# Kernel optimization log

Measured on AMD Instinct MI355X. Metric: run time of the kernel, lower is better.

The kernel has to match this reference:

```python
import jax, jax.numpy as jnp
import numpy as np

B, L, C = 2, 384, 128
H, DK, NQP, NPV = 8, 16, 4, 8
WC = float(np.sqrt(2.0 / (9.0 * NQP)))
WL = float(np.sqrt(1.0 / 3.0))


def setup_inputs() -> dict:
    key = jax.random.key(0)
    ks = jax.random.split(key, 16)
    s = 0.02
    inp = {
        "si": jax.random.normal(ks[0], (B, L, C), jnp.float32),
        "zij": jax.random.normal(ks[1], (B, L, L, C), jnp.float32),
        "Ri": jax.random.normal(ks[2], (B, L, 3, 3), jnp.float32),
        "Ti": jax.random.normal(ks[3], (B, L, 3, 1), jnp.float32),
        "WQh": jax.random.normal(ks[4], (C, H * DK), jnp.float32) * s,
        "WKh": jax.random.normal(ks[5], (C, H * DK), jnp.float32) * s,
        "WVh": jax.random.normal(ks[6], (C, H * DK), jnp.float32) * s,
        "WQhp": jax.random.normal(ks[7], (C, H * NQP * 3), jnp.float32) * s,
        "WKhp": jax.random.normal(ks[8], (C, H * NQP * 3), jnp.float32) * s,
        "WVhp": jax.random.normal(ks[9], (C, H * NPV * 3), jnp.float32) * s,
        "Wb": jax.random.normal(ks[10], (C, H), jnp.float32) * s,
        "WOw": jax.random.normal(ks[11], (H * C + H * DK + H * NPV * 3 + H * NPV, C), jnp.float32) * s,
        "WOb": jnp.zeros((C,), jnp.float32),
        "gamah": jnp.zeros((H,), jnp.float32),
    }
    return inp


def reference(si, zij, Ri, Ti, WQh, WKh, WVh, WQhp, WKhp, WVhp, Wb, WOw, WOb, gamah):
    b, l, c = si.shape
    t = Ti[..., 0]  # [B,L,3]

    # scalar q/k/v: [B,L,H,DK]
    q = (si @ WQh).reshape(b, l, H, DK)
    k = (si @ WKh).reshape(b, l, H, DK)
    v = (si @ WVh).reshape(b, l, H, DK)

    # pair bias: [B,H,L,L]
    bij = jnp.einsum("bijc,ch->bhij", zij, Wb)
    scores1 = jnp.einsum("bihd,bjhd->bhij", q, k) / np.sqrt(DK) + bij

    # query/key points, rigid-transformed: [B,L,H,P,3]
    qp = (si @ WQhp).reshape(b, l, H, NQP, 3)
    kp = (si @ KHP_shape_fix(WKhp)).reshape(b, l, H, NQP, 3) if False else (si @ WKhp).reshape(b, l, H, NQP, 3)
    qpt = jnp.einsum("bixy,bihpy->bihpx", Ri, qp) + t[:, :, None, None, :]
    kpt = jnp.einsum("bixy,bihpy->bihpx", Ri, kp) + t[:, :, None, None, :]

    # squared point distances summed over points and coords, via |q|^2+|k|^2-2qk
    sq_q = jnp.sum(qpt * qpt, axis=(-1, -2))  # [B,L,H]
    sq_k = jnp.sum(kpt * kpt, axis=(-1, -2))  # [B,L,H]
    dot = jnp.einsum("bihpx,bjhpx->bhij", qpt, kpt)
    d2 = sq_q.transpose(0, 2, 1)[:, :, :, None] + sq_k.transpose(0, 2, 1)[:, :, None, :] - 2.0 * dot

    scores2 = jax.nn.softplus(gamah)[None, :, None, None] * (WC / 2.0) * d2
    scores = WL * (scores1 - scores2)
    alphah = jax.nn.softmax(scores, axis=3)  # [B,H,L,L]

    # pair-rep aggregation: [B,L,H,C]
    o_pair = jnp.einsum("bhij,bijc->bihc", alphah, zij)
    # scalar value attention: [B,L,H,DK]
    o_val = jnp.einsum("bhij,bjhd->bihd", alphah, v)

    # point values, transformed, attended, then inverse-transformed
    vp = (si @ WVhp).reshape(b, l, H, NPV, 3)
    vpt = jnp.einsum("bjxy,bjhpy->bjhpx", Ri, vp) + t[:, :, None, None, :]
    opt = jnp.einsum("bhij,bjhpx->bihpx", alphah, vpt)  # [B,L,H,NPV,3]
    ohp = jnp.einsum("binm,bihpn->bihpm", Ri, opt - t[:, :, None, None, :])  # R^T (o - t)

    feats = jnp.concatenate(
        [
            o_pair.reshape(b, l, H * c),
            o_val.reshape(b, l, H * DK),
            ohp.reshape(b, l, H * NPV * 3),
            jnp.abs(ohp).sum(axis=-1).reshape(b, l, H * NPV),
        ],
        axis=2,
    )
    return feats @ WOw + WOb


def KHP_shape_fix(w):  # unused placeholder kept for readability of the conditional above
    return w
```

## Files before the change

kernel.cpp:

```cpp
#include <hip/hip_runtime.h>
#include <hip/hip_bf16.h>

#define Bq 2
#define Lq 384
#define Cq 128
#define Hq 8

static constexpr float WCH   = 0.11785113019775792f;
static constexpr float WLc   = 0.5773502691896258f;
static constexpr float LOG2E = 1.4426950408889634f;

typedef __attribute__((ext_vector_type(8))) short bf16x8;
typedef __attribute__((ext_vector_type(4))) float f32x4;

__device__ __forceinline__ unsigned short f2bf(float f) {
  __hip_bfloat16 h = __float2bfloat16(f);
  unsigned short u; __builtin_memcpy(&u, &h, 2); return u;
}
__device__ __forceinline__ unsigned packbf(float a, float b) {
  return (unsigned)f2bf(a) | ((unsigned)f2bf(b) << 16);
}
__device__ __forceinline__ float bf2f(unsigned short u) {
  unsigned x = ((unsigned)u) << 16; float f; __builtin_memcpy(&f, &x, 4); return f;
}
__device__ __forceinline__ bf16x8 ld_frag(const unsigned* p) {
  union { bf16x8 v; unsigned u[4]; } x;
  x.u[0] = p[0]; x.u[1] = p[1]; x.u[2] = p[2]; x.u[3] = p[3];
  return x.v;
}

#define BAR() asm volatile("s_waitcnt lgkmcnt(0)\ns_barrier" ::: "memory")

__global__ __launch_bounds__(256) void k_proj(
    const float* __restrict__ si,
    const float* __restrict__ WQh, const float* __restrict__ WKh, const float* __restrict__ WVh,
    const float* __restrict__ WQhp, const float* __restrict__ WKhp, const float* __restrict__ WVhp,
    float* __restrict__ q, float* __restrict__ k, float* __restrict__ v,
    float* __restrict__ raw)
{
  __shared__ unsigned sm[4352*2];
  unsigned* at = sm;
  unsigned* bt = sm + 4352;
  unsigned short* bt16 = (unsigned short*)bt;
  const int t = threadIdx.x;
  const int tb = blockIdx.x / 12, ct = blockIdx.x % 12;
  const int tok0 = tb*64, cg0 = ct*64;

  {
    const float4* sp = (const float4*)si;
    #pragma unroll
    for (int rep = 0; rep < 8; ++rep) {
      int idx = rep*256 + t;
      int tl = idx >> 5, cq = idx & 31;
      float4 vv = sp[(size_t)(tok0+tl)*32 + cq];
      uint2 u; u.x = packbf(vv.x, vv.y); u.y = packbf(vv.z, vv.w);
      *(uint2*)(&at[tl*68 + cq*2]) = u;
    }
  }
  {
    const int cq = t & 15;
    const int cg = cg0 + cq*4;
    const float* Wsrc; int ncol, coff;
    if (cg < 128)      { Wsrc = WQh; ncol = 128; coff = cg; }
    else if (cg < 256) { Wsrc = WKh; ncol = 128; coff = cg-128; }
    else if (cg < 384) { Wsrc = WVh; ncol = 128; coff = cg-256; }
    else { int pc = cg-384;
      if (pc < 96)       { Wsrc = WQhp; ncol = 96;  coff = pc; }
      else if (pc < 192) { Wsrc = WKhp; ncol = 96;  coff = pc-96; }
      else               { Wsrc = WVhp; ncol = 192; coff = pc-192; } }
    #pragma unroll
    for (int rep = 0; rep < 8; ++rep) {
      int c = rep*16 + (t >> 4);
      float4 wv = *(const float4*)(Wsrc + (size_t)c*ncol + coff);
      bt16[(cq*4+0)*136 + c] = f2bf(wv.x);
      bt16[(cq*4+1)*136 + c] = f2bf(wv.y);
      bt16[(cq*4+2)*136 + c] = f2bf(wv.z);
      bt16[(cq*4+3)*136 + c] = f2bf(wv.w);
    }
  }
  __syncthreads();
  const int l = t & 63, w = t >> 6, g = l >> 4, n16 = l & 15;
  bf16x8 afr[4];
  #pragma unroll
  for (int ks = 0; ks < 4; ++ks)
    afr[ks] = ld_frag(&at[(w*16 + n16)*68 + ks*16 + g*4]);
  f32x4 acc[4];
  #pragma unroll
  for (int nl = 0; nl < 4; ++nl) { acc[nl][0]=0.f; acc[nl][1]=0.f; acc[nl][2]=0.f; acc[nl][3]=0.f; }
  #pragma unroll
  for (int nl = 0; nl < 4; ++nl)
    #pragma unroll
    for (int ks = 0; ks < 4; ++ks) {
      bf16x8 bfr = ld_frag(&bt[(nl*16 + n16)*68 + ks*16 + g*4]);
      acc[nl] = __builtin_amdgcn_mfma_f32_16x16x32_bf16(afr[ks], bfr, acc[nl], 0, 0, 0);
    }
  if (ct < 6) {
    float* dst = (ct < 2) ? q : (ct < 4) ? k : v;
    int colbase = cg0 - (ct >> 1)*128;
    #pragma unroll
    for (int nl = 0; nl < 4; ++nl)
      #pragma unroll
      for (int r = 0; r < 4; ++r)
        dst[(size_t)(tok0 + w*16 + g*4 + r)*128 + colbase + nl*16 + n16] = acc[nl][r];
  } else {
    int pcb = cg0 - 384;
    #pragma unroll
    for (int nl = 0; nl < 4; ++nl)
      #pragma unroll
      for (int r = 0; r < 4; ++r)
        raw[(size_t)(tok0 + w*16 + g*4 + r)*384 + pcb + nl*16 + n16] = acc[nl][r];
  }
}

__global__ __launch_bounds__(256) void k_xform(
    const float* __restrict__ raw, const float* __restrict__ Ri, const float* __restrict__ Ti,
    const float* __restrict__ qg, const float* __restrict__ kg, const float* __restrict__ gamah,
    float* __restrict__ vpt, unsigned* __restrict__ apk, unsigned* __restrict__ bpk)
{
  __shared__ float ssq[128];
  __shared__ float spt[2][64][3];
  __shared__ float smsq[2][2][8];
  const int t = threadIdx.x;
  const int tk = t >> 7, pt = t & 127;
  const int tok = blockIdx.x*2 + tk;
  {
    const float* R = Ri + tok*9;
    const float* T = Ti + tok*3;
    int ro = (pt < 32) ? pt*3 : (pt < 64) ? 96 + (pt-32)*3 : 192 + (pt-64)*3;
    float x0 = raw[(size_t)tok*384 + ro + 0], x1 = raw[(size_t)tok*384 + ro + 1], x2 = raw[(size_t)tok*384 + ro + 2];
    float o0 = T[0] + R[0]*x0 + R[1]*x1 + R[2]*x2;
    float o1 = T[1] + R[3]*x0 + R[4]*x1 + R[5]*x2;
    float o2 = T[2] + R[6]*x0 + R[7]*x1 + R[8]*x2;
    if (pt >= 64) {
      int doff = tok*192 + (pt-64)*3;
      vpt[doff] = o0; vpt[doff+1] = o1; vpt[doff+2] = o2;
    } else {
      spt[tk][pt][0] = o0; spt[tk][pt][1] = o1; spt[tk][pt][2] = o2;
      ssq[tk*64 + pt] = o0*o0 + o1*o1 + o2*o2;
    }
  }
  __syncthreads();
  if (t < 32) {
    int tk2 = t >> 4, r = t & 15, isK = r >> 3, h = r & 7;
    int base = tk2*64 + isK*32 + h*4;
    smsq[tk2][isK][h] = ssq[base] + ssq[base+1] + ssq[base+2] + ssq[base+3];
  }
  __syncthreads();
  {
    const int ab = t >> 7, rem = t & 127;
    const int tk2 = rem >> 6, h = (rem >> 3) & 7, d0 = (t & 7)*2;
    const int tokg = blockIdx.x*2 + tk2;
    float gv = gamah[h];
    float sp = (gv > 20.f) ? gv : log1pf(__expf(gv));
    float c1 = WLc*0.25f, c2 = 2.f*WLc*sp*WCH, c3 = WLc*sp*WCH;
    unsigned* dst = (ab ? bpk : apk) + ((size_t)tokg*8 + h)*16;
    #pragma unroll
    for (int dd = 0; dd < 2; ++dd) {
      int dw = d0 + dd;
      float vv[2];
      #pragma unroll
      for (int e = 0; e < 2; ++e) {
        int kk = dw*2 + e;
        float val;
        if (kk < 16)      val = (ab ? kg : qg)[(size_t)tokg*128 + h*16 + kk] * (ab ? 1.f : c1);
        else if (kk < 28) { int pi = kk-16;
                            float cv = spt[tk2][ab*32 + h*4 + pi/3][pi%3];
                            val = ab ? cv : cv*c2; }
        else if (kk == 28) val = ab ? 1.f : -c3*smsq[tk2][0][h];
        else if (kk == 29) val = ab ? smsq[tk2][1][h] : -c3;
        else               val = 0.f;
        vv[e] = val;
      }
      dst[dw] = packbf(vv[0], vv[1]);
    }
  }
}

__global__ __launch_bounds__(256) void k_geom(
    const unsigned* __restrict__ apk, const unsigned* __restrict__ bpk,
    float* __restrict__ g)
{
  __shared__ unsigned bt[384*20];
  const int t = threadIdx.x;
  const int bh = blockIdx.x / 6, ib = blockIdx.x % 6;
  const int b = bh >> 3, h = bh & 7, i0 = ib*64;
  #pragma unroll
  for (int rep = 0; rep < 6; ++rep) {
    int idx = rep*256 + t;
    int j = idx >> 2, dq = idx & 3;
    uint4 vv = *(const uint4*)(bpk + ((size_t)(b*Lq + j)*8 + h)*16 + dq*4);
    *(uint4*)(&bt[j*20 + dq*4]) = vv;
  }
  __syncthreads();
  const int l = t & 63, w = t >> 6, g2 = l >> 4, n16 = l & 15;
  union { uint4 u; bf16x8 v; } au;
  au.u = *(const uint4*)(apk + ((size_t)(b*Lq + i0 + w*16 + n16)*8 + h)*16 + g2*4);
  bf16x8 afr = au.v;
  float* grow = g + (size_t)(b*8 + h)*Lq*Lq;
  for (int jt = 0; jt < 24; ++jt) {
    bf16x8 bfr = ld_frag(&bt[(jt*16 + n16)*20 + g2*4]);
    f32x4 acc = {0.f,0.f,0.f,0.f};
    acc = __builtin_amdgcn_mfma_f32_16x16x32_bf16(afr, bfr, acc, 0, 0, 0);
    #pragma unroll
    for (int r = 0; r < 4; ++r)
      grow[(size_t)(i0 + w*16 + g2*4 + r)*Lq + jt*16 + n16] = acc[r];
  }
}

#define ZS   0
#define ZT   4352
#define GS   8832
#define P2O  11936
#define WBT  12496
#define WMX  13568
#define LSM  13632
#define SCL  13696
#define INV  13704
#define OPTS 13712
#define OS   13904
#define SMTOT 14928

__global__ __launch_bounds__(256, 2) void k_attn(
    const float* __restrict__ zij, const float* __restrict__ gmat,
    const float* __restrict__ v, const float* __restrict__ vpt,
    const float* __restrict__ Wb, const float* __restrict__ Ri, const float* __restrict__ Ti,
    float* __restrict__ feats)
{
  __shared__ unsigned sm[SMTOT];
  float* smf = (float*)sm;
  const int t = threadIdx.x;
  const int bx = blockIdx.x;
  const int b = bx / Lq, i = bx % Lq;
  const int tok = bx;
  const int l = t & 63, w = t >> 6, g = l >> 4, hh = l & 15;

  {
    const float* gp = gmat + (size_t)(b*8)*Lq*Lq + (size_t)i*Lq;
    #pragma unroll
    for (int rep = 0; rep < 3; ++rep) {
      int idx = rep*256 + t;
      int h2 = idx / 96, jq = idx % 96;
      float4 gv = *(const float4*)(gp + (size_t)h2*Lq*Lq + jq*4);
      *(float4*)(&smf[GS + h2*388 + jq*4]) = gv;
    }
    unsigned short* wb16 = (unsigned short*)(sm + WBT);
    #pragma unroll
    for (int rep = 0; rep < 8; ++rep) {
      int idx = rep*256 + t;
      int h2 = idx >> 7, c = idx & 127;
      wb16[h2*134 + c] = (h2 < 8) ? f2bf(Wb[c*8 + h2]) : (unsigned short)0;
    }
  }
  __syncthreads();
  bf16x8 wbf[4];
  #pragma unroll
  for (int ks = 0; ks < 4; ++ks) wbf[ks] = ld_frag(&sm[WBT + hh*67 + ks*16 + g*4]);

  f32x4 opacc0 = {0.f,0.f,0.f,0.f}, opacc1 = {0.f,0.f,0.f,0.f};
  float m_run = -1e30f, l_run = 0.f;
  float va0 = 0.f, va1 = 0.f;
  int role_h = 0; const float* rp = nullptr; int rstride = 0;
  if (t < 64)       { role_h = t >> 3; rp = v   + (size_t)b*Lq*128 + role_h*16 + (t & 7)*2; rstride = 128; }
  else if (t < 160) { int qq = t - 64; role_h = qq / 12;
                      rp = vpt + (size_t)b*Lq*192 + role_h*24 + (qq % 12)*2; rstride = 192; }

  const int c4 = t & 31, jr = t >> 5;
  const float4* zp = (const float4*)(zij + (size_t)tok*Lq*128);
  unsigned short* zt16 = (unsigned short*)(sm + ZT);
  float4 zr[8];
  #pragma unroll
  for (int pp = 0; pp < 8; ++pp) zr[pp] = zp[(size_t)(pp*8 + jr)*32 + c4];

  for (int ch = 0; ch < 6; ++ch) {
    const int j0 = ch*64;
    BAR();
    #pragma unroll
    for (int pp = 0; pp < 8; ++pp) {
      int j = pp*8 + jr;
      uint2 u; u.x = packbf(zr[pp].x, zr[pp].y); u.y = packbf(zr[pp].z, zr[pp].w);
      *(uint2*)(&sm[ZS + j*68 + c4*2]) = u;
      zt16[(c4*4+0)*70 + j] = (unsigned short)(u.x & 0xffffu);
      zt16[(c4*4+1)*70 + j] = (unsigned short)(u.x >> 16);
      zt16[(c4*4+2)*70 + j] = (unsigned short)(u.y & 0xffffu);
      zt16[(c4*4+3)*70 + j] = (unsigned short)(u.y >> 16);
    }
    if (ch < 5) {
      #pragma unroll
      for (int pp = 0; pp < 8; ++pp)
        zr[pp] = zp[(size_t)(j0 + 64 + pp*8 + jr)*32 + c4];
    }
    BAR();
    f32x4 bij = {0.f,0.f,0.f,0.f};
    #pragma unroll
    for (int ks = 0; ks < 4; ++ks) {
      bf16x8 a = ld_frag(&sm[ZS + (w*16 + hh)*68 + ks*16 + g*4]);
      bij = __builtin_amdgcn_mfma_f32_16x16x32_bf16(a, wbf[ks], bij, 0, 0, 0);
    }
    float s0, s1, s2, s3;
    if (hh < 8) {
      f32x4 gq = *(const f32x4*)(&smf[GS + hh*388 + j0 + w*16 + g*4]);
      s0 = gq[0] + WLc*bij[0]; s1 = gq[1] + WLc*bij[1];
      s2 = gq[2] + WLc*bij[2]; s3 = gq[3] + WLc*bij[3];
    } else { s0 = s1 = s2 = s3 = -1e30f; }
    float m4 = fmaxf(fmaxf(s0,s1), fmaxf(s2,s3));
    m4 = fmaxf(m4, __shfl_xor(m4, 16));
    m4 = fmaxf(m4, __shfl_xor(m4, 32));
    if (l < 16) smf[WMX + w*16 + l] = m4;
    BAR();
    float cmax = fmaxf(fmaxf(smf[WMX+hh], smf[WMX+16+hh]),
                       fmaxf(smf[WMX+32+hh], smf[WMX+48+hh]));
    float m_new = fmaxf(m_run, cmax);
    float sc = exp2f((m_run - m_new)*LOG2E);
    m_run = m_new;
    float p0 = exp2f((s0 - m_new)*LOG2E);
    float p1 = exp2f((s1 - m_new)*LOG2E);
    float p2 = exp2f((s2 - m_new)*LOG2E);
    float p3 = exp2f((s3 - m_new)*LOG2E);
    float psum = p0+p1+p2+p3;
    psum += __shfl_xor(psum, 16);
    psum += __shfl_xor(psum, 32);
    l_run = l_run*sc + psum;
    sm[P2O + hh*35 + w*8 + g*2    ] = packbf(p0, p1);
    sm[P2O + hh*35 + w*8 + g*2 + 1] = packbf(p2, p3);
    opacc0 = opacc0 * sc;
    opacc1 = opacc1 * sc;
    if (w == 0 && l < 8) smf[SCL + l] = sc;
    BAR();
    #pragma unroll
    for (int ks = 0; ks < 2; ++ks) {
      bf16x8 bb = ld_frag(&sm[P2O + hh*35 + ks*16 + g*4]);
      bf16x8 a0 = ld_frag(&sm[ZT + ((w  )*16 + hh)*35 + ks*16 + g*4]);
      bf16x8 a1 = ld_frag(&sm[ZT + ((w+4)*16 + hh)*35 + ks*16 + g*4]);
      opacc0 = __builtin_amdgcn_mfma_f32_16x16x32_bf16(a0, bb, opacc0, 0, 0, 0);
      opacc1 = __builtin_amdgcn_mfma_f32_16x16x32_bf16(a1, bb, opacc1, 0, 0, 0);
    }
    if (t < 160) {
      float scl = smf[SCL + role_h];
      va0 *= scl; va1 *= scl;
      #pragma unroll 4
      for (int jj = 0; jj < 64; jj += 2) {
        unsigned pw = sm[P2O + role_h*35 + (jj>>1)];
        float pa = bf2f((unsigned short)(pw & 0xffffu));
        float pb = bf2f((unsigned short)(pw >> 16));
        const float* pj = rp + (size_t)(j0+jj)*rstride;
        const float* pk2 = pj + rstride;
        va0 += pa*pj[0] + pb*pk2[0];
        va1 += pa*pj[1] + pb*pk2[1];
      }
    }
  }
  __syncthreads();
  if (l < 16) smf[LSM + w*16 + l] = l_run;
  __syncthreads();
  if (t < 8) {
    float lt = smf[LSM+t] + smf[LSM+16+t] + smf[LSM+32+t] + smf[LSM+48+t];
    smf[INV + t] = 1.f / lt;
  }
  __syncthreads();
  const size_t fb = (size_t)tok * 1408;
  if (hh < 8) {
    float inv = smf[INV + hh];
    #pragma unroll
    for (int r = 0; r < 4; ++r) {
      smf[OS + hh*128 + (w  )*16 + g*4 + r] = opacc0[r]*inv;
      smf[OS + hh*128 + (w+4)*16 + g*4 + r] = opacc1[r]*inv;
    }
  }
  if (t < 64) {
    float inv = smf[INV + role_h];
    int off = role_h*16 + (t & 7)*2;
    feats[fb + 1024 + off    ] = va0*inv;
    feats[fb + 1024 + off + 1] = va1*inv;
  } else if (t < 160) {
    float inv = smf[INV + role_h];
    int qq = t - 64;
    smf[OPTS + role_h*24 + (qq%12)*2    ] = va0*inv;
    smf[OPTS + role_h*24 + (qq%12)*2 + 1] = va1*inv;
  }
  __syncthreads();
  for (int rep = 0; rep < 4; ++rep) {
    int idx = rep*256 + t;
    feats[fb + idx] = smf[OS + idx];
  }
  if (t < 64) {
    int h2 = t >> 3, p = t & 7;
    const float* R = Ri + tok*9;
    const float* T = Ti + tok*3;
    float ox = smf[OPTS + h2*24 + p*3 + 0] - T[0];
    float oy = smf[OPTS + h2*24 + p*3 + 1] - T[1];
    float oz = smf[OPTS + h2*24 + p*3 + 2] - T[2];
    float r0 = R[0]*ox + R[3]*oy + R[6]*oz;
    float r1 = R[1]*ox + R[4]*oy + R[7]*oz;
    float r2 = R[2]*ox + R[5]*oy + R[8]*oz;
    feats[fb + 1152 + (h2*8+p)*3 + 0] = r0;
    feats[fb + 1152 + (h2*8+p)*3 + 1] = r1;
    feats[fb + 1152 + (h2*8+p)*3 + 2] = r2;
    feats[fb + 1344 + h2*8 + p] = fabsf(r0) + fabsf(r1) + fabsf(r2);
  }
}

__global__ __launch_bounds__(256) void k_out(
    const float* __restrict__ feats, const float* __restrict__ WOw,
    const float* __restrict__ WOb, float* __restrict__ out)
{
  __shared__ float sf[8448];
  const int t = threadIdx.x;
  const int r0 = blockIdx.x * 6;
  for (int rep = 0; rep < 33; ++rep) {
    int idx = rep*256 + t;
    int row = idx / 1408, f = idx % 1408;
    sf[f*6 + row] = feats[(size_t)(r0+row)*1408 + f];
  }
  __syncthreads();
  const int c4 = t & 31, fq = t >> 5;
  float acc[6][4];
  #pragma unroll
  for (int r = 0; r < 6; ++r)
    #pragma unroll
    for (int e = 0; e < 4; ++e) acc[r][e] = 0.f;
  const float* wp = WOw + (size_t)fq*176*128 + c4*4;
  for (int f = 0; f < 176; ++f) {
    const f32x4 wv = *(const f32x4*)(wp + (size_t)f*128);
    int fg = fq*176 + f;
    float fv[6];
    #pragma unroll
    for (int r = 0; r < 6; ++r) fv[r] = sf[fg*6 + r];
    #pragma unroll
    for (int r = 0; r < 6; ++r)
      #pragma unroll
      for (int e = 0; e < 4; ++e) acc[r][e] += fv[r]*wv[e];
  }
  __syncthreads();
  #pragma unroll
  for (int r = 0; r < 6; ++r)
    #pragma unroll
    for (int e = 0; e < 4; ++e)
      sf[(fq*6 + r)*128 + c4*4 + e] = acc[r][e];
  __syncthreads();
  for (int rep = 0; rep < 3; ++rep) {
    int idx = rep*256 + t;
    int r = idx >> 7, cc = idx & 127;
    float s = 0.f;
    #pragma unroll
    for (int fq2 = 0; fq2 < 8; ++fq2) s += sf[(fq2*6 + r)*128 + cc];
    out[(size_t)(r0+r)*128 + cc] = s + WOb[cc];
  }
}

extern "C" void kernel_launch(void* const* d_in, const int* in_sizes, int n_in,
                              void* d_out, int out_size, void* d_ws, size_t ws_size,
                              hipStream_t stream) {
  const float* si    = (const float*)d_in[0];
  const float* zij   = (const float*)d_in[1];
  const float* Ri    = (const float*)d_in[2];
  const float* Ti    = (const float*)d_in[3];
  const float* WQh   = (const float*)d_in[4];
  const float* WKh   = (const float*)d_in[5];
  const float* WVh   = (const float*)d_in[6];
  const float* WQhp  = (const float*)d_in[7];
  const float* WKhp  = (const float*)d_in[8];
  const float* WVhp  = (const float*)d_in[9];
  const float* Wb    = (const float*)d_in[10];
  const float* WOw   = (const float*)d_in[11];
  const float* WOb   = (const float*)d_in[12];
  const float* gamah = (const float*)d_in[13];

  float* ws   = (float*)d_ws;
  float* q    = ws;
  float* k    = q    + 98304;
  float* v    = k    + 98304;
  float* vpt  = v    + 98304;
  float* raw  = vpt  + 147456;
  float* g    = raw  + 294912;
  float* feats= g    + 2359296;
  unsigned* apk = (unsigned*)feats;
  unsigned* bpk = apk + 98304;
  float* out  = (float*)d_out;

  k_proj <<<144, 256, 0, stream>>>(si, WQh, WKh, WVh, WQhp, WKhp, WVhp, q, k, v, raw);
  k_xform<<<384, 256, 0, stream>>>(raw, Ri, Ti, q, k, gamah, vpt, apk, bpk);
  k_geom <<<96,  256, 0, stream>>>(apk, bpk, g);
  k_attn <<<768, 256, 0, stream>>>(zij, g, v, vpt, Wb, Ri, Ti, feats);
  k_out  <<<128, 256, 0, stream>>>(feats, WOw, WOb, out);
}
```

Measured before the change: 314.4 us.

## Move value and point-value attention onto fp16 MFMA with transposed staged operands

Every matrix op switches from bf16 to fp16 MFMA. The scalar-value and point-value aggregation in the attention kernel moves from per-thread scalar FMA loops over global memory onto MFMA. To feed it, v and the transformed value points are written as transposed fp16 arrays, prefetched per chunk alongside zij and staged in shared memory. The pair-bias g rows are now held in registers instead of shared memory, and per-row softmax rescale factors are tracked for the new accumulators. This aims to remove the scalar global-load bottleneck in k_attn, at the cost of more registers and shared memory, and fp16 range and precision risk.

```diff
diff --git a/kernel.cpp b/kernel.cpp
--- a/kernel.cpp
+++ b/kernel.cpp
@@ -10,21 +10,18 @@
 static constexpr float WLc   = 0.5773502691896258f;
 static constexpr float LOG2E = 1.4426950408889634f;
 
-typedef __attribute__((ext_vector_type(8))) short bf16x8;
+typedef __fp16 f16x8 __attribute__((ext_vector_type(8)));
 typedef __attribute__((ext_vector_type(4))) float f32x4;
 
-__device__ __forceinline__ unsigned short f2bf(float f) {
-  __hip_bfloat16 h = __float2bfloat16(f);
-  unsigned short u; __builtin_memcpy(&u, &h, 2); return u;
-}
-__device__ __forceinline__ unsigned packbf(float a, float b) {
-  return (unsigned)f2bf(a) | ((unsigned)f2bf(b) << 16);
-}
-__device__ __forceinline__ float bf2f(unsigned short u) {
-  unsigned x = ((unsigned)u) << 16; float f; __builtin_memcpy(&f, &x, 4); return f;
-}
-__device__ __forceinline__ bf16x8 ld_frag(const unsigned* p) {
-  union { bf16x8 v; unsigned u[4]; } x;
+__device__ __forceinline__ unsigned short f2h(float f) {
+  __fp16 h = (__fp16)f; unsigned short u; __builtin_memcpy(&u, &h, 2); return u;
+}
+__device__ __forceinline__ unsigned packh(float a, float b) {
+  auto v = __builtin_amdgcn_cvt_pkrtz(a, b);
+  unsigned u; __builtin_memcpy(&u, &v, 4); return u;
+}
+__device__ __forceinline__ f16x8 ld_frag16(const unsigned* p) {
+  union { f16x8 v; unsigned u[4]; } x;
   x.u[0] = p[0]; x.u[1] = p[1]; x.u[2] = p[2]; x.u[3] = p[3];
   return x.v;
 }
@@ -35,7 +32,7 @@
     const float* __restrict__ si,
     const float* __restrict__ WQh, const float* __restrict__ WKh, const float* __restrict__ WVh,
     const float* __restrict__ WQhp, const float* __restrict__ WKhp, const float* __restrict__ WVhp,
-    float* __restrict__ q, float* __restrict__ k, float* __restrict__ v,
+    float* __restrict__ q, float* __restrict__ k, unsigned short* __restrict__ vt_g,
     float* __restrict__ raw)
 {
   __shared__ unsigned sm[4352*2];
@@ -53,7 +50,7 @@
       int idx = rep*256 + t;
       int tl = idx >> 5, cq = idx & 31;
       float4 vv = sp[(size_t)(tok0+tl)*32 + cq];
-      uint2 u; u.x = packbf(vv.x, vv.y); u.y = packbf(vv.z, vv.w);
+      uint2 u; u.x = packh(vv.x, vv.y); u.y = packh(vv.z, vv.w);
       *(uint2*)(&at[tl*68 + cq*2]) = u;
     }
   }
@@ -72,18 +69,18 @@
     for (int rep = 0; rep < 8; ++rep) {
       int c = rep*16 + (t >> 4);
       float4 wv = *(const float4*)(Wsrc + (size_t)c*ncol + coff);
-      bt16[(cq*4+0)*136 + c] = f2bf(wv.x);
-      bt16[(cq*4+1)*136 + c] = f2bf(wv.y);
-      bt16[(cq*4+2)*136 + c] = f2bf(wv.z);
-      bt16[(cq*4+3)*136 + c] = f2bf(wv.w);
+      bt16[(cq*4+0)*136 + c] = f2h(wv.x);
+      bt16[(cq*4+1)*136 + c] = f2h(wv.y);
+      bt16[(cq*4+2)*136 + c] = f2h(wv.z);
+      bt16[(cq*4+3)*136 + c] = f2h(wv.w);
     }
   }
   __syncthreads();
   const int l = t & 63, w = t >> 6, g = l >> 4, n16 = l & 15;
-  bf16x8 afr[4];
+  f16x8 afr[4];
   #pragma unroll
   for (int ks = 0; ks < 4; ++ks)
-    afr[ks] = ld_frag(&at[(w*16 + n16)*68 + ks*16 + g*4]);
+    afr[ks] = ld_frag16(&at[(w*16 + n16)*68 + ks*16 + g*4]);
   f32x4 acc[4];
   #pragma unroll
   for (int nl = 0; nl < 4; ++nl) { acc[nl][0]=0.f; acc[nl][1]=0.f; acc[nl][2]=0.f; acc[nl][3]=0.f; }
@@ -91,17 +88,24 @@
   for (int nl = 0; nl < 4; ++nl)
     #pragma unroll
     for (int ks = 0; ks < 4; ++ks) {
-      bf16x8 bfr = ld_frag(&bt[(nl*16 + n16)*68 + ks*16 + g*4]);
-      acc[nl] = __builtin_amdgcn_mfma_f32_16x16x32_bf16(afr[ks], bfr, acc[nl], 0, 0, 0);
-    }
-  if (ct < 6) {
-    float* dst = (ct < 2) ? q : (ct < 4) ? k : v;
+      f16x8 bfr = ld_frag16(&bt[(nl*16 + n16)*68 + ks*16 + g*4]);
+      acc[nl] = __builtin_amdgcn_mfma_f32_16x16x32_f16(afr[ks], bfr, acc[nl], 0, 0, 0);
+    }
+  if (ct < 4) {
+    float* dst = (ct < 2) ? q : k;
     int colbase = cg0 - (ct >> 1)*128;
     #pragma unroll
     for (int nl = 0; nl < 4; ++nl)
       #pragma unroll
       for (int r = 0; r < 4; ++r)
         dst[(size_t)(tok0 + w*16 + g*4 + r)*128 + colbase + nl*16 + n16] = acc[nl][r];
+  } else if (ct < 6) {
+    int colbase = cg0 - 256;
+    #pragma unroll
+    for (int nl = 0; nl < 4; ++nl)
+      #pragma unroll
+      for (int r = 0; r < 4; ++r)
+        vt_g[(size_t)(colbase + nl*16 + n16)*768 + tok0 + w*16 + g*4 + r] = f2h(acc[nl][r]);
   } else {
     int pcb = cg0 - 384;
     #pragma unroll
@@ -115,7 +119,7 @@
 __global__ __launch_bounds__(256) void k_xform(
     const float* __restrict__ raw, const float* __restrict__ Ri, const float* __restrict__ Ti,
     const float* __restrict__ qg, const float* __restrict__ kg, const float* __restrict__ gamah,
-    float* __restrict__ vpt, unsigned* __restrict__ apk, unsigned* __restrict__ bpk)
+    unsigned short* __restrict__ vptt, unsigned* __restrict__ apk, unsigned* __restrict__ bpk)
 {
   __shared__ float ssq[128];
   __shared__ float spt[2][64][3];
@@ -132,8 +136,10 @@
     float o1 = T[1] + R[3]*x0 + R[4]*x1 + R[5]*x2;
     float o2 = T[2] + R[6]*x0 + R[7]*x1 + R[8]*x2;
     if (pt >= 64) {
-      int doff = tok*192 + (pt-64)*3;
-      vpt[doff] = o0; vpt[doff+1] = o1; vpt[doff+2] = o2;
+      int col = (pt-64)*3;
+      vptt[(size_t)(col+0)*768 + tok] = f2h(o0);
+      vptt[(size_t)(col+1)*768 + tok] = f2h(o1);
+      vptt[(size_t)(col+2)*768 + tok] = f2h(o2);
     } else {
       spt[tk][pt][0] = o0; spt[tk][pt][1] = o1; spt[tk][pt][2] = o2;
       ssq[tk*64 + pt] = o0*o0 + o1*o1 + o2*o2;
@@ -171,7 +177,7 @@
         else               val = 0.f;
         vv[e] = val;
       }
-      dst[dw] = packbf(vv[0], vv[1]);
+      dst[dw] = packh(vv[0], vv[1]);
     }
   }
 }
@@ -193,122 +199,161 @@
   }
   __syncthreads();
   const int l = t & 63, w = t >> 6, g2 = l >> 4, n16 = l & 15;
-  union { uint4 u; bf16x8 v; } au;
+  union { uint4 u; f16x8 v; } au;
   au.u = *(const uint4*)(apk + ((size_t)(b*Lq + i0 + w*16 + n16)*8 + h)*16 + g2*4);
-  bf16x8 afr = au.v;
+  f16x8 afr = au.v;
   float* grow = g + (size_t)(b*8 + h)*Lq*Lq;
   for (int jt = 0; jt < 24; ++jt) {
-    bf16x8 bfr = ld_frag(&bt[(jt*16 + n16)*20 + g2*4]);
+    f16x8 bfr = ld_frag16(&bt[(jt*16 + n16)*20 + g2*4]);
     f32x4 acc = {0.f,0.f,0.f,0.f};
-    acc = __builtin_amdgcn_mfma_f32_16x16x32_bf16(afr, bfr, acc, 0, 0, 0);
+    acc = __builtin_amdgcn_mfma_f32_16x16x32_f16(afr, bfr, acc, 0, 0, 0);
     #pragma unroll
     for (int r = 0; r < 4; ++r)
       grow[(size_t)(i0 + w*16 + g2*4 + r)*Lq + jt*16 + n16] = acc[r];
   }
 }
 
-#define ZS   0
-#define ZT   4352
-#define GS   8832
-#define P2O  11936
-#define WBT  12496
-#define WMX  13568
-#define LSM  13632
-#define SCL  13696
-#define INV  13704
-#define OPTS 13712
-#define OS   13904
-#define SMTOT 14928
+#define ZSo   0
+#define ZTo   4224
+#define VTo   8704
+#define VPo   12928
+#define P2o   19264
+#define WBo   19824
+#define WMo   20368
+#define INVo  20432
+#define SMTOT 20440
+#define OPo   0
+#define OSo   8704
 
 __global__ __launch_bounds__(256, 2) void k_attn(
     const float* __restrict__ zij, const float* __restrict__ gmat,
-    const float* __restrict__ v, const float* __restrict__ vpt,
+    const unsigned short* __restrict__ vt_g, const unsigned short* __restrict__ vptt,
     const float* __restrict__ Wb, const float* __restrict__ Ri, const float* __restrict__ Ti,
     float* __restrict__ feats)
 {
   __shared__ unsigned sm[SMTOT];
   float* smf = (float*)sm;
+  unsigned short* zt16 = (unsigned short*)(sm + ZTo);
   const int t = threadIdx.x;
   const int bx = blockIdx.x;
   const int b = bx / Lq, i = bx % Lq;
-  const int tok = bx;
   const int l = t & 63, w = t >> 6, g = l >> 4, hh = l & 15;
 
+  const int c4 = t & 31, jr = t >> 5;
+  const float4* zp = (const float4*)(zij + (size_t)bx*Lq*128);
+  float4 zr[8];
+  #pragma unroll
+  for (int pp = 0; pp < 8; ++pp) zr[pp] = zp[(size_t)(pp*8 + jr)*32 + c4];
+  const uint4* vtp = (const uint4*)vt_g;
+  const uint4* vpp = (const uint4*)vptt;
+  uint4 vtr[4], vpr[6];
+  #pragma unroll
+  for (int q2 = 0; q2 < 4; ++q2) {
+    int u = q2*256 + t, row = u >> 3, seg = u & 7;
+    vtr[q2] = vtp[row*96 + b*48 + seg];
+  }
+  #pragma unroll
+  for (int q2 = 0; q2 < 6; ++q2) {
+    int u = q2*256 + t, row = u >> 3, seg = u & 7;
+    vpr[q2] = vpp[row*96 + b*48 + seg];
+  }
+
+  f32x4 greg[6];
+  #pragma unroll
+  for (int ch = 0; ch < 6; ++ch) { greg[ch][0]=0.f; greg[ch][1]=0.f; greg[ch][2]=0.f; greg[ch][3]=0.f; }
+  if (hh < 8) {
+    const float* gp = gmat + ((size_t)(b*8 + hh)*Lq + i)*Lq;
+    #pragma unroll
+    for (int ch = 0; ch < 6; ++ch)
+      greg[ch] = *(const f32x4*)(gp + ch*64 + w*16 + g*4);
+  }
+
   {
-    const float* gp = gmat + (size_t)(b*8)*Lq*Lq + (size_t)i*Lq;
-    #pragma unroll
-    for (int rep = 0; rep < 3; ++rep) {
+    unsigned short* wb16 = (unsigned short*)(sm + WBo);
+    #pragma unroll
+    for (int rep = 0; rep < 4; ++rep) {
       int idx = rep*256 + t;
-      int h2 = idx / 96, jq = idx % 96;
-      float4 gv = *(const float4*)(gp + (size_t)h2*Lq*Lq + jq*4);
-      *(float4*)(&smf[GS + h2*388 + jq*4]) = gv;
-    }
-    unsigned short* wb16 = (unsigned short*)(sm + WBT);
-    #pragma unroll
-    for (int rep = 0; rep < 8; ++rep) {
-      int idx = rep*256 + t;
-      int h2 = idx >> 7, c = idx & 127;
-      wb16[h2*134 + c] = (h2 < 8) ? f2bf(Wb[c*8 + h2]) : (unsigned short)0;
-    }
-  }
-  __syncthreads();
-  bf16x8 wbf[4];
-  #pragma unroll
-  for (int ks = 0; ks < 4; ++ks) wbf[ks] = ld_frag(&sm[WBT + hh*67 + ks*16 + g*4]);
+      int c = idx >> 3, h2 = idx & 7;
+      wb16[h2*136 + c] = f2h(Wb[c*8 + h2]);
+    }
+  }
+  __syncthreads();
+  const f16x8 zf8 = {0,0,0,0,0,0,0,0};
+  f16x8 wbf[4];
+  #pragma unroll
+  for (int ks = 0; ks < 4; ++ks)
+    wbf[ks] = (hh < 8) ? ld_frag16(&sm[WBo + hh*68 + ks*16 + g*4]) : zf8;
 
   f32x4 opacc0 = {0.f,0.f,0.f,0.f}, opacc1 = {0.f,0.f,0.f,0.f};
+  f32x4 anv0 = {0.f,0.f,0.f,0.f}, anv1 = {0.f,0.f,0.f,0.f};
+  f32x4 apv0 = {0.f,0.f,0.f,0.f}, apv1 = {0.f,0.f,0.f,0.f}, apv2 = {0.f,0.f,0.f,0.f};
   float m_run = -1e30f, l_run = 0.f;
-  float va0 = 0.f, va1 = 0.f;
-  int role_h = 0; const float* rp = nullptr; int rstride = 0;
-  if (t < 64)       { role_h = t >> 3; rp = v   + (size_t)b*Lq*128 + role_h*16 + (t & 7)*2; rstride = 128; }
-  else if (t < 160) { int qq = t - 64; role_h = qq / 12;
-                      rp = vpt + (size_t)b*Lq*192 + role_h*24 + (qq % 12)*2; rstride = 192; }
-
-  const int c4 = t & 31, jr = t >> 5;
-  const float4* zp = (const float4*)(zij + (size_t)tok*Lq*128);
-  unsigned short* zt16 = (unsigned short*)(sm + ZT);
-  float4 zr[8];
-  #pragma unroll
-  for (int pp = 0; pp < 8; ++pp) zr[pp] = zp[(size_t)(pp*8 + jr)*32 + c4];
+  float mr0 = -1e30f, mr1 = -1e30f, mr2 = -1e30f, mr3 = -1e30f;
 
   for (int ch = 0; ch < 6; ++ch) {
-    const int j0 = ch*64;
     BAR();
     #pragma unroll
     for (int pp = 0; pp < 8; ++pp) {
       int j = pp*8 + jr;
-      uint2 u; u.x = packbf(zr[pp].x, zr[pp].y); u.y = packbf(zr[pp].z, zr[pp].w);
-      *(uint2*)(&sm[ZS + j*68 + c4*2]) = u;
-      zt16[(c4*4+0)*70 + j] = (unsigned short)(u.x & 0xffffu);
-      zt16[(c4*4+1)*70 + j] = (unsigned short)(u.x >> 16);
-      zt16[(c4*4+2)*70 + j] = (unsigned short)(u.y & 0xffffu);
-      zt16[(c4*4+3)*70 + j] = (unsigned short)(u.y >> 16);
+      unsigned u0 = packh(zr[pp].x, zr[pp].y), u1 = packh(zr[pp].z, zr[pp].w);
+      uint2 u; u.x = u0; u.y = u1;
+      *(uint2*)(&sm[ZSo + j*66 + c4*2]) = u;
+      zt16[(c4*4+0)*70 + j] = (unsigned short)(u0 & 0xffffu);
+      zt16[(c4*4+1)*70 + j] = (unsigned short)(u0 >> 16);
+      zt16[(c4*4+2)*70 + j] = (unsigned short)(u1 & 0xffffu);
+      zt16[(c4*4+3)*70 + j] = (unsigned short)(u1 >> 16);
+    }
+    #pragma unroll
+    for (int q2 = 0; q2 < 4; ++q2) {
+      int u = q2*256 + t, row = u >> 3, seg = u & 7;
+      sm[VTo + row*33 + seg*4    ] = vtr[q2].x;
+      sm[VTo + row*33 + seg*4 + 1] = vtr[q2].y;
+      sm[VTo + row*33 + seg*4 + 2] = vtr[q2].z;
+      sm[VTo + row*33 + seg*4 + 3] = vtr[q2].w;
+    }
+    #pragma unroll
+    for (int q2 = 0; q2 < 6; ++q2) {
+      int u = q2*256 + t, row = u >> 3, seg = u & 7;
+      sm[VPo + row*33 + seg*4    ] = vpr[q2].x;
+      sm[VPo + row*33 + seg*4 + 1] = vpr[q2].y;
+      sm[VPo + row*33 + seg*4 + 2] = vpr[q2].z;
+      sm[VPo + row*33 + seg*4 + 3] = vpr[q2].w;
     }
     if (ch < 5) {
+      int j0n = (ch+1)*64;
       #pragma unroll
       for (int pp = 0; pp < 8; ++pp)
-        zr[pp] = zp[(size_t)(j0 + 64 + pp*8 + jr)*32 + c4];
+        zr[pp] = zp[(size_t)(j0n + pp*8 + jr)*32 + c4];
+      #pragma unroll
+      for (int q2 = 0; q2 < 4; ++q2) {
+        int u = q2*256 + t, row = u >> 3, seg = u & 7;
+        vtr[q2] = vtp[row*96 + b*48 + (ch+1)*8 + seg];
+      }
+      #pragma unroll
+      for (int q2 = 0; q2 < 6; ++q2) {
+        int u = q2*256 + t, row = u >> 3, seg = u & 7;
+        vpr[q2] = vpp[row*96 + b*48 + (ch+1)*8 + seg];
+      }
     }
     BAR();
     f32x4 bij = {0.f,0.f,0.f,0.f};
     #pragma unroll
     for (int ks = 0; ks < 4; ++ks) {
-      bf16x8 a = ld_frag(&sm[ZS + (w*16 + hh)*68 + ks*16 + g*4]);
-      bij = __builtin_amdgcn_mfma_f32_16x16x32_bf16(a, wbf[ks], bij, 0, 0, 0);
+      f16x8 a = ld_frag16(&sm[ZSo + (w*16 + hh)*66 + ks*16 + g*4]);
+      bij = __builtin_amdgcn_mfma_f32_16x16x32_f16(a, wbf[ks], bij, 0, 0, 0);
     }
     float s0, s1, s2, s3;
     if (hh < 8) {
-      f32x4 gq = *(const f32x4*)(&smf[GS + hh*388 + j0 + w*16 + g*4]);
-      s0 = gq[0] + WLc*bij[0]; s1 = gq[1] + WLc*bij[1];
-      s2 = gq[2] + WLc*bij[2]; s3 = gq[3] + WLc*bij[3];
+      s0 = greg[ch][0] + WLc*bij[0]; s1 = greg[ch][1] + WLc*bij[1];
+      s2 = greg[ch][2] + WLc*bij[2]; s3 = greg[ch][3] + WLc*bij[3];
     } else { s0 = s1 = s2 = s3 = -1e30f; }
     float m4 = fmaxf(fmaxf(s0,s1), fmaxf(s2,s3));
     m4 = fmaxf(m4, __shfl_xor(m4, 16));
     m4 = fmaxf(m4, __shfl_xor(m4, 32));
-    if (l < 16) smf[WMX + w*16 + l] = m4;
+    if (l < 16) smf[WMo + w*16 + l] = m4;
     BAR();
-    float cmax = fmaxf(fmaxf(smf[WMX+hh], smf[WMX+16+hh]),
-                       fmaxf(smf[WMX+32+hh], smf[WMX+48+hh]));
+    float cmax = fmaxf(fmaxf(smf[WMo+hh], smf[WMo+16+hh]),
+                       fmaxf(smf[WMo+32+hh], smf[WMo+48+hh]));
     float m_new = fmaxf(m_run, cmax);
     float sc = exp2f((m_run - m_new)*LOG2E);
     m_run = m_new;
@@ -320,75 +365,99 @@
     psum += __shfl_xor(psum, 16);
     psum += __shfl_xor(psum, 32);
     l_run = l_run*sc + psum;
-    sm[P2O + hh*35 + w*8 + g*2    ] = packbf(p0, p1);
-    sm[P2O + hh*35 + w*8 + g*2 + 1] = packbf(p2, p3);
+    sm[P2o + hh*35 + w*8 + g*2    ] = packh(p0, p1);
+    sm[P2o + hh*35 + w*8 + g*2 + 1] = packh(p2, p3);
+    float scr0, scr1, scr2, scr3;
+    {
+      int hr = g*4;
+      float cm, mn;
+      cm = fmaxf(fmaxf(smf[WMo+hr], smf[WMo+16+hr]), fmaxf(smf[WMo+32+hr], smf[WMo+48+hr]));
+      mn = fmaxf(mr0, cm); scr0 = exp2f((mr0 - mn)*LOG2E); mr0 = mn;
+      cm = fmaxf(fmaxf(smf[WMo+hr+1], smf[WMo+17+hr]), fmaxf(smf[WMo+33+hr], smf[WMo+49+hr]));
+      mn = fmaxf(mr1, cm); scr1 = exp2f((mr1 - mn)*LOG2E); mr1 = mn;
+      cm = fmaxf(fmaxf(smf[WMo+hr+2], smf[WMo+18+hr]), fmaxf(smf[WMo+34+hr], smf[WMo+50+hr]));
+      mn = fmaxf(mr2, cm); scr2 = exp2f((mr2 - mn)*LOG2E); mr2 = mn;
+      cm = fmaxf(fmaxf(smf[WMo+hr+3], smf[WMo+19+hr]), fmaxf(smf[WMo+35+hr], smf[WMo+51+hr]));
+      mn = fmaxf(mr3, cm); scr3 = exp2f((mr3 - mn)*LOG2E); mr3 = mn;
+    }
     opacc0 = opacc0 * sc;
     opacc1 = opacc1 * sc;
-    if (w == 0 && l < 8) smf[SCL + l] = sc;
+    anv0[0]*=scr0; anv0[1]*=scr1; anv0[2]*=scr2; anv0[3]*=scr3;
+    anv1[0]*=scr0; anv1[1]*=scr1; anv1[2]*=scr2; anv1[3]*=scr3;
+    apv0[0]*=scr0; apv0[1]*=scr1; apv0[2]*=scr2; apv0[3]*=scr3;
+    apv1[0]*=scr0; apv1[1]*=scr1; apv1[2]*=scr2; apv1[3]*=scr3;
+    apv2[0]*=scr0; apv2[1]*=scr1; apv2[2]*=scr2; apv2[3]*=scr3;
     BAR();
     #pragma unroll
     for (int ks = 0; ks < 2; ++ks) {
-      bf16x8 bb = ld_frag(&sm[P2O + hh*35 + ks*16 + g*4]);
-      bf16x8 a0 = ld_frag(&sm[ZT + ((w  )*16 + hh)*35 + ks*16 + g*4]);
-      bf16x8 a1 = ld_frag(&sm[ZT + ((w+4)*16 + hh)*35 + ks*16 + g*4]);
-      opacc0 = __builtin_amdgcn_mfma_f32_16x16x32_bf16(a0, bb, opacc0, 0, 0, 0);
-      opacc1 = __builtin_amdgcn_mfma_f32_16x16x32_bf16(a1, bb, opacc1, 0, 0, 0);
-    }
-    if (t < 160) {
-      float scl = smf[SCL + role_h];
-      va0 *= scl; va1 *= scl;
-      #pragma unroll 4
-      for (int jj = 0; jj < 64; jj += 2) {
-        unsigned pw = sm[P2O + role_h*35 + (jj>>1)];
-        float pa = bf2f((unsigned short)(pw & 0xffffu));
-        float pb = bf2f((unsigned short)(pw >> 16));
-        const float* pj = rp + (size_t)(j0+jj)*rstride;
-        const float* pk2 = pj + rstride;
-        va0 += pa*pj[0] + pb*pk2[0];
-        va1 += pa*pj[1] + pb*pk2[1];
-      }
-    }
-  }
-  __syncthreads();
-  if (l < 16) smf[LSM + w*16 + l] = l_run;
+      f16x8 bb = ld_frag16(&sm[P2o + hh*35 + ks*16 + g*4]);
+      f16x8 a0 = ld_frag16(&sm[ZTo + ((w  )*16 + hh)*35 + ks*16 + g*4]);
+      f16x8 a1 = ld_frag16(&sm[ZTo + ((w+4)*16 + hh)*35 + ks*16 + g*4]);
+      opacc0 = __builtin_amdgcn_mfma_f32_16x16x32_f16(a0, bb, opacc0, 0, 0, 0);
+      opacc1 = __builtin_amdgcn_mfma_f32_16x16x32_f16(a1, bb, opacc1, 0, 0, 0);
+      f16x8 v0 = ld_frag16(&sm[VTo + ((2*w  )*16 + hh)*33 + ks*16 + g*4]);
+      f16x8 v1 = ld_frag16(&sm[VTo + ((2*w+1)*16 + hh)*33 + ks*16 + g*4]);
+      anv0 = __builtin_amdgcn_mfma_f32_16x16x32_f16(bb, v0, anv0, 0, 0, 0);
+      anv1 = __builtin_amdgcn_mfma_f32_16x16x32_f16(bb, v1, anv1, 0, 0, 0);
+      f16x8 p0f = ld_frag16(&sm[VPo + ((3*w  )*16 + hh)*33 + ks*16 + g*4]);
+      f16x8 p1f = ld_frag16(&sm[VPo + ((3*w+1)*16 + hh)*33 + ks*16 + g*4]);
+      f16x8 p2f = ld_frag16(&sm[VPo + ((3*w+2)*16 + hh)*33 + ks*16 + g*4]);
+      apv0 = __builtin_amdgcn_mfma_f32_16x16x32_f16(bb, p0f, apv0, 0, 0, 0);
+      apv1 = __builtin_amdgcn_mfma_f32_16x16x32_f16(bb, p1f, apv1, 0, 0, 0);
+      apv2 = __builtin_amdgcn_mfma_f32_16x16x32_f16(bb, p2f, apv2, 0, 0, 0);
+    }
+  }
+  __syncthreads();
+  if (l < 16) smf[WMo + w*16 + l] = l_run;
   __syncthreads();
   if (t < 8) {
-    float lt = smf[LSM+t] + smf[LSM+16+t] + smf[LSM+32+t] + smf[LSM+48+t];
-    smf[INV + t] = 1.f / lt;
-  }
-  __syncthreads();
-  const size_t fb = (size_t)tok * 1408;
+    float lt = smf[WMo+t] + smf[WMo+16+t] + smf[WMo+32+t] + smf[WMo+48+t];
+    smf[INVo + t] = 1.f / lt;
+  }
+  __syncthreads();
+  const size_t fb = (size_t)bx * 1408;
   if (hh < 8) {
-    float inv = smf[INV + hh];
+    float inv = smf[INVo + hh];
     #pragma unroll
     for (int r = 0; r < 4; ++r) {
-      smf[OS + hh*128 + (w  )*16 + g*4 + r] = opacc0[r]*inv;
-      smf[OS + hh*128 + (w+4)*16 + g*4 + r] = opacc1[r]*inv;
-    }
-  }
-  if (t < 64) {
-    float inv = smf[INV + role_h];
-    int off = role_h*16 + (t & 7)*2;
-    feats[fb + 1024 + off    ] = va0*inv;
-    feats[fb + 1024 + off + 1] = va1*inv;
-  } else if (t < 160) {
-    float inv = smf[INV + role_h];
-    int qq = t - 64;
-    smf[OPTS + role_h*24 + (qq%12)*2    ] = va0*inv;
-    smf[OPTS + role_h*24 + (qq%12)*2 + 1] = va1*inv;
-  }
-  __syncthreads();
+      smf[OSo + hh*128 + (w  )*16 + g*4 + r] = opacc0[r]*inv;
+      smf[OSo + hh*128 + (w+4)*16 + g*4 + r] = opacc1[r]*inv;
+    }
+  }
+  {
+    int nt0 = 2*w;
+    if (g == (nt0 >> 2))
+      feats[fb + 1024 + nt0*16 + hh] = anv0[nt0 & 3] * smf[INVo + nt0];
+    int nt1 = 2*w + 1;
+    if (g == (nt1 >> 2))
+      feats[fb + 1024 + nt1*16 + hh] = anv1[nt1 & 3] * smf[INVo + nt1];
+  }
+  #pragma unroll
+  for (int ti = 0; ti < 3; ++ti) {
+    int col = (3*w + ti)*16 + hh;
+    int h2 = col / 24;
+    float val = 0.f;
+    #pragma unroll
+    for (int r = 0; r < 4; ++r) {
+      float av = (ti == 0) ? apv0[r] : (ti == 1) ? apv1[r] : apv2[r];
+      if (h2 == g*4 + r) val = av;
+    }
+    if (h2 >= g*4 && h2 < g*4 + 4)
+      smf[OPo + col] = val * smf[INVo + h2];
+  }
+  __syncthreads();
+  #pragma unroll
   for (int rep = 0; rep < 4; ++rep) {
     int idx = rep*256 + t;
-    feats[fb + idx] = smf[OS + idx];
+    feats[fb + idx] = smf[OSo + idx];
   }
   if (t < 64) {
     int h2 = t >> 3, p = t & 7;
-    const float* R = Ri + tok*9;
-    const float* T = Ti + tok*3;
-    float ox = smf[OPTS + h2*24 + p*3 + 0] - T[0];
-    float oy = smf[OPTS + h2*24 + p*3 + 1] - T[1];
-    float oz = smf[OPTS + h2*24 + p*3 + 2] - T[2];
+    const float* R = Ri + bx*9;
+    const float* T = Ti + bx*3;
+    float ox = smf[OPo + h2*24 + p*3 + 0] - T[0];
+    float oy = smf[OPo + h2*24 + p*3 + 1] - T[1];
+    float oz = smf[OPo + h2*24 + p*3 + 2] - T[2];
     float r0 = R[0]*ox + R[3]*oy + R[6]*oz;
     float r1 = R[1]*ox + R[4]*oy + R[7]*oz;
     float r2 = R[2]*ox + R[5]*oy + R[8]*oz;
@@ -467,19 +536,19 @@
 
   float* ws   = (float*)d_ws;
   float* q    = ws;
-  float* k    = q    + 98304;
-  float* v    = k    + 98304;
-  float* vpt  = v    + 98304;
-  float* raw  = vpt  + 147456;
-  float* g    = raw  + 294912;
-  float* feats= g    + 2359296;
+  float* k    = q + 98304;
+  float* raw  = k + 98304;
+  float* g    = raw + 294912;
+  float* feats= g + 2359296;
+  unsigned short* vt_g = (unsigned short*)(feats + 1081344);
+  unsigned short* vptt = vt_g + 98304;
   unsigned* apk = (unsigned*)feats;
   unsigned* bpk = apk + 98304;
   float* out  = (float*)d_out;
 
-  k_proj <<<144, 256, 0, stream>>>(si, WQh, WKh, WVh, WQhp, WKhp, WVhp, q, k, v, raw);
-  k_xform<<<384, 256, 0, stream>>>(raw, Ri, Ti, q, k, gamah, vpt, apk, bpk);
+  k_proj <<<144, 256, 0, stream>>>(si, WQh, WKh, WVh, WQhp, WKhp, WVhp, q, k, vt_g, raw);
+  k_xform<<<384, 256, 0, stream>>>(raw, Ri, Ti, q, k, gamah, vptt, apk, bpk);
   k_geom <<<96,  256, 0, stream>>>(apk, bpk, g);
-  k_attn <<<768, 256, 0, stream>>>(zij, g, v, vpt, Wb, Ri, Ti, feats);
+  k_attn <<<768, 256, 0, stream>>>(zij, g, vt_g, vptt, Wb, Ri, Ti, feats);
   k_out  <<<128, 256, 0, stream>>>(feats, WOw, WOb, out);
 }
```

New measurement: 290.5 us. -7.6%, faster.
